# Kernel optimization log

Hardware: AMD Instinct MI355X
Metric: run time of the kernel (lower is better)

The kernel has to match this reference:

```python
import jax, jax.numpy as jnp
import numpy as np

H = 128        # hidden_dim
NP = 512       # program nodes
NV = 50000     # voxel nodes
E = 800000     # cross edges (16 per voxel)
TAU = 1.0
SLOPE = 0.01   # LeakyReLU default negative slope


def setup_inputs() -> dict:
    key = jax.random.key(0)
    ks = jax.random.split(key, 12)
    s = 1.0 / np.sqrt(H)
    x = jax.random.normal(ks[0], (NP, H), dtype=jnp.float32)
    v = jax.random.normal(ks[1], (NV, H), dtype=jnp.float32)
    row0 = jax.random.randint(ks[2], (E,), 0, NP, dtype=jnp.int32)
    row1 = (jnp.arange(E, dtype=jnp.int32) % NV)  # every voxel gets E/NV edges
    cross_edge_index = jnp.stack([row0, row1])    # [2, E]
    W_program = jax.random.normal(ks[3], (H, H), dtype=jnp.float32) * s
    b_program = jnp.zeros((H,), dtype=jnp.float32)
    W_voxel = jax.random.normal(ks[4], (H, H), dtype=jnp.float32) * s
    b_voxel = jnp.zeros((H,), dtype=jnp.float32)
    W_m1 = jax.random.normal(ks[5], (H, H), dtype=jnp.float32) * s
    b_m1 = jnp.zeros((H,), dtype=jnp.float32)
    W_m2 = jax.random.normal(ks[6], (H, 1), dtype=jnp.float32) * s
    b_m2 = jnp.zeros((1,), dtype=jnp.float32)
    theta = jax.random.normal(ks[7], (H, 1), dtype=jnp.float32) * s  # xavier-like
    u = jax.random.uniform(ks[8], (E,), dtype=jnp.float32)
    gumbel_u = jnp.clip(u, 1e-7, 1.0 - 1e-7)  # avoid log(0)
    return {"x": x, "v": v, "cross_edge_index": cross_edge_index,
            "W_program": W_program, "b_program": b_program,
            "W_voxel": W_voxel, "b_voxel": b_voxel,
            "W_m1": W_m1, "b_m1": b_m1, "W_m2": W_m2, "b_m2": b_m2,
            "theta": theta, "gumbel_u": gumbel_u}


def reference(x, v, cross_edge_index, W_program, b_program, W_voxel, b_voxel,
              W_m1, b_m1, W_m2, b_m2, theta, gumbel_u):
    src = cross_edge_index[0]
    dst = cross_edge_index[1]
    x_sel = x[src]                      # [E, H] gather
    v_sel = v[dst]                      # [E, H] gather
    # mask = sigmoid(MLP(v)) : Linear -> LeakyReLU -> Linear(H,1)
    a = v @ W_m1 + b_m1
    a = jnp.where(a >= 0, a, SLOPE * a)
    mask = jax.nn.sigmoid(a @ W_m2 + b_m2)                  # [NV, 1]
    # attention logits: theta^T * tanh(Wp x_sel + Wv v_sel), summed over H
    t = jnp.tanh(x_sel @ W_program + b_program + v_sel @ W_voxel + b_voxel)
    e = jnp.sum(t * theta[:, 0], axis=-1)                   # [E]
    # Gumbel softmax: global softmax over all edges (dim=0 in torch on 1-D e)
    g = -jnp.log(-jnp.log(gumbel_u))
    y = jax.nn.softmax((e + g) / TAU)                       # [E]
    # per-voxel hard argmax (scatter_max), straight-through estimator
    seg_max = jax.ops.segment_max(y, dst, num_segments=NV)  # [NV]
    is_max = y == seg_max[dst]
    cand = jnp.where(is_max, jnp.arange(E), E)
    argmax = jax.ops.segment_min(cand, dst, num_segments=NV)  # [NV], first max per voxel
    y_hard_1 = jnp.zeros(E + 1, y.dtype).at[argmax].set(1.0)[:E]  # overflow slot for empty segments
    y_hard = jax.lax.stop_gradient(y_hard_1 - y) + y
    # scatter-sum of soft-attended program features back to voxels
    summed = jax.ops.segment_sum(x_sel * y[:, None], dst, num_segments=NV)  # [NV, H]
    v_out = v + mask * summed
    return (v_out, mask, y[:, None], y_hard[:, None])
```

## Files before the change

### kernel.cpp

```cpp
#include <hip/hip_runtime.h>

#define H     128
#define NP    512
#define NVOX  50000
#define NEDGE 800000
#define EPV   16
#define SLOPE 0.01f
#define GR    32
#define NBLK  1563
#define STRH  136
#define VSTR  132
#define C1    2.8853900817779268f
#define LOG2E 1.4426950408889634f
#define ABLK  3125

#define EXP2(x) __builtin_amdgcn_exp2f(x)
#define LOG2(x) __builtin_amdgcn_logf(x)
#define RCP(x)  __builtin_amdgcn_rcpf(x)

typedef _Float16 h16;
typedef __attribute__((ext_vector_type(4))) _Float16 h16x4;
typedef __attribute__((ext_vector_type(8))) _Float16 h16x8;
typedef __attribute__((ext_vector_type(4))) float    f32x4;

__global__ __launch_bounds__(256) void k_pre(const float* __restrict__ x,
                                             const float* __restrict__ Wp,
                                             const float* __restrict__ bp,
                                             const float* __restrict__ Wv,
                                             const float* __restrict__ Wm1,
                                             float* __restrict__ xpout,
                                             h16* __restrict__ WvThi,
                                             h16* __restrict__ WvTlo,
                                             h16* __restrict__ Wm1T) {
    __shared__ float part[H];
    int bid = blockIdx.x;
    int tid = threadIdx.x;
    if (bid < NP) {
        int row = bid;
        int col = tid & 127;
        int kh  = tid >> 7;
        int kbase = kh * 64;
        const float* xr = x + (size_t)row * H;
        float acc = 0.f;
#pragma unroll 8
        for (int k = 0; k < 64; ++k)
            acc = fmaf(xr[kbase + k], Wp[(size_t)(kbase + k) * H + col], acc);
        if (kh == 1) part[col] = acc;
        __syncthreads();
        if (kh == 0) xpout[(size_t)row * H + col] = (acc + part[col] + bp[col]) * C1;
    } else {
        int idx = (bid - NP) * 256 + tid;
        if (idx < 16384) {
            int k = idx >> 7, n = idx & 127;
            float w = Wv[idx];
            h16 hi = (h16)w;
            WvThi[n * H + k] = hi;
            WvTlo[n * H + k] = (h16)(w - (float)hi);
        } else {
            int j = idx - 16384;
            int k = j >> 7, n = j & 127;
            Wm1T[n * H + k] = (h16)Wm1[j];
        }
    }
}

__global__ __launch_bounds__(256, 4) void k_mainX(
    const float* __restrict__ v,   const float* __restrict__ x,
    const float* __restrict__ bv,  const float* __restrict__ bm1,
    const float* __restrict__ Wm2, const float* __restrict__ bm2,
    const h16* __restrict__ WvThi, const h16* __restrict__ WvTlo,
    const h16* __restrict__ Wm1T,
    const float* __restrict__ xp,  const int* __restrict__ cei,
    const float* __restrict__ theta, const float* __restrict__ gum,
    float* __restrict__ mask_out, float* __restrict__ pout,
    float* __restrict__ sump,     float* __restrict__ partial)
{
    __shared__ __align__(16) char ldsbuf[2 * GR * STRH * 2];
    h16*   vh = (h16*)ldsbuf;
    h16*   vl = vh + GR * STRH;
    float* vt = (float*)ldsbuf;
    __shared__ float ptile[EPV * GR];
    __shared__ int   ceit[EPV * GR];
    __shared__ float gumt[EPV * GR];
    __shared__ int   amtile[GR];
    __shared__ float pmbuf[4][GR];
    __shared__ float psums[4];

    int tid  = threadIdx.x;
    int base = blockIdx.x * GR;

#pragma unroll
    for (int i = 0; i < 4; ++i) {
        int f  = i * 256 + tid;
        int r  = f >> 5, c4 = f & 31;
        int gr = base + r; if (gr >= NVOX) gr = NVOX - 1;
        float4 val = *(const float4*)&v[(size_t)gr * H + c4 * 4];
        h16x4 hi, lo;
        hi.x = (h16)val.x; lo.x = (h16)(val.x - (float)hi.x);
        hi.y = (h16)val.y; lo.y = (h16)(val.y - (float)hi.y);
        hi.z = (h16)val.z; lo.z = (h16)(val.z - (float)hi.z);
        hi.w = (h16)val.w; lo.w = (h16)(val.w - (float)hi.w);
        *(h16x4*)&vh[r * STRH + c4 * 4] = hi;
        *(h16x4*)&vl[r * STRH + c4 * 4] = lo;
    }
#pragma unroll
    for (int it = 0; it < 2; ++it) {
        int idx = it * 256 + tid;
        int t = idx >> 5, c = idx & 31;
        int vx = base + c; if (vx >= NVOX) vx = NVOX - 1;
        int e = vx + t * NVOX;
        ceit[idx] = cei[e];
        gumt[idx] = gum[e];
    }
    __syncthreads();

    int wave = tid >> 6, lane = tid & 63;
    int m16 = lane & 15, quad = lane >> 4;
    int cb = wave * 32;

    f32x4 aV[2][2], aM[2][2];
#pragma unroll
    for (int rt = 0; rt < 2; ++rt)
#pragma unroll
        for (int ct = 0; ct < 2; ++ct) { aV[rt][ct] = (f32x4)0.f; aM[rt][ct] = (f32x4)0.f; }

#pragma unroll
    for (int kc = 0; kc < 4; ++kc) {
        int kofs = kc * 32 + quad * 8;
        h16x8 ah[2], al[2];
#pragma unroll
        for (int rt = 0; rt < 2; ++rt) {
            int row = rt * 16 + m16;
            ah[rt] = *(const h16x8*)&vh[row * STRH + kofs];
            al[rt] = *(const h16x8*)&vl[row * STRH + kofs];
        }
#pragma unroll
        for (int ct = 0; ct < 2; ++ct) {
            int n = cb + ct * 16 + m16;
            h16x8 bh = *(const h16x8*)&WvThi[n * H + kofs];
            h16x8 bl = *(const h16x8*)&WvTlo[n * H + kofs];
            h16x8 bm = *(const h16x8*)&Wm1T[n * H + kofs];
#pragma unroll
            for (int rt = 0; rt < 2; ++rt) {
                aV[rt][ct] = __builtin_amdgcn_mfma_f32_16x16x32_f16(ah[rt], bh, aV[rt][ct], 0, 0, 0);
                aV[rt][ct] = __builtin_amdgcn_mfma_f32_16x16x32_f16(al[rt], bh, aV[rt][ct], 0, 0, 0);
                aV[rt][ct] = __builtin_amdgcn_mfma_f32_16x16x32_f16(ah[rt], bl, aV[rt][ct], 0, 0, 0);
                aM[rt][ct] = __builtin_amdgcn_mfma_f32_16x16x32_f16(ah[rt], bm, aM[rt][ct], 0, 0, 0);
            }
        }
    }
    __syncthreads();

    float pml[2][4];
#pragma unroll
    for (int rt = 0; rt < 2; ++rt)
#pragma unroll
        for (int reg = 0; reg < 4; ++reg) pml[rt][reg] = 0.f;
#pragma unroll
    for (int ct = 0; ct < 2; ++ct) {
        int col = cb + ct * 16 + m16;
        float bvc = bv[col], bmc = bm1[col], w2c = Wm2[col];
#pragma unroll
        for (int rt = 0; rt < 2; ++rt)
#pragma unroll
            for (int reg = 0; reg < 4; ++reg) {
                int row = rt * 16 + quad * 4 + reg;
                vt[row * VSTR + col] = (aV[rt][ct][reg] + bvc) * C1;
                float m = aM[rt][ct][reg] + bmc;
                m = (m >= 0.f) ? m : SLOPE * m;
                pml[rt][reg] = fmaf(m, w2c, pml[rt][reg]);
            }
    }
#pragma unroll
    for (int off = 8; off >= 1; off >>= 1)
#pragma unroll
        for (int rt = 0; rt < 2; ++rt)
#pragma unroll
            for (int reg = 0; reg < 4; ++reg)
                pml[rt][reg] += __shfl_xor(pml[rt][reg], off, 64);
    if (m16 == 0) {
#pragma unroll
        for (int rt = 0; rt < 2; ++rt)
#pragma unroll
            for (int reg = 0; reg < 4; ++reg)
                pmbuf[wave][rt * 16 + quad * 4 + reg] = pml[rt][reg];
    }
    __syncthreads();
    if (wave == 0 && lane < GR) {
        int gr = base + lane;
        if (gr < NVOX) {
            float s = pmbuf[0][lane] + pmbuf[1][lane] + pmbuf[2][lane]
                    + pmbuf[3][lane] + bm2[0];
            mask_out[gr] = RCP(1.f + EXP2(-s * LOG2E));
        }
    }

    int g = tid >> 3, lk = tid & 7;
    int vox = base + g;
    bool valid = vox < NVOX;
    float th2[16], thsum = 0.f;
#pragma unroll
    for (int i = 0; i < 4; ++i) {
        float4 t4 = *(const float4*)&theta[(lk + 8 * i) * 4];
        th2[i * 4 + 0] = -2.f * LOG2E * t4.x; th2[i * 4 + 1] = -2.f * LOG2E * t4.y;
        th2[i * 4 + 2] = -2.f * LOG2E * t4.z; th2[i * 4 + 3] = -2.f * LOG2E * t4.w;
        thsum += LOG2E * (t4.x + t4.y + t4.z + t4.w);
    }
    const float* vr = &vt[g * VSTR];
    float4 b0 = *(const float4*)&vr[(lk +  0) * 4];
    float4 b1 = *(const float4*)&vr[(lk +  8) * 4];
    float4 b2 = *(const float4*)&vr[(lk + 16) * 4];
    float4 b3 = *(const float4*)&vr[(lk + 24) * 4];

    float4 s0 = make_float4(0.f,0.f,0.f,0.f), s1 = s0, s2 = s0, s3 = s0;
    float psum = 0.f, pmax = -1.f;
    int   pidx = 0;

    int srcC = ceit[g];
    const float4* xr0 = (const float4*)(xp + (size_t)srcC * H);
    float4 a0 = xr0[lk], a1 = xr0[lk + 8], a2 = xr0[lk + 16], a3 = xr0[lk + 24];

    for (int t = 0; t < EPV; ++t) {
        float4 n0, n1, n2, n3;
        int srcN;
        if (t < EPV - 1) {
            srcN = ceit[(t + 1) * GR + g];
            const float4* xrN = (const float4*)(xp + (size_t)srcN * H);
            n0 = xrN[lk]; n1 = xrN[lk + 8]; n2 = xrN[lk + 16]; n3 = xrN[lk + 24];
        } else {
            srcN = srcC; n0 = a0; n1 = a1; n2 = a2; n3 = a3;
        }
        const float4* xo = (const float4*)(x + (size_t)srcC * H);
        float4 c0 = xo[lk], c1 = xo[lk + 8], c2 = xo[lk + 16], c3 = xo[lk + 24];
        float wvt = -LOG2E * RCP(LOG2(gumt[t * GR + g]));

        float acc0 = thsum, acc1 = 0.f;
        acc0 = fmaf(th2[ 0], RCP(EXP2(a0.x + b0.x) + 1.f), acc0);
        acc1 = fmaf(th2[ 1], RCP(EXP2(a0.y + b0.y) + 1.f), acc1);
        acc0 = fmaf(th2[ 2], RCP(EXP2(a0.z + b0.z) + 1.f), acc0);
        acc1 = fmaf(th2[ 3], RCP(EXP2(a0.w + b0.w) + 1.f), acc1);
        acc0 = fmaf(th2[ 4], RCP(EXP2(a1.x + b1.x) + 1.f), acc0);
        acc1 = fmaf(th2[ 5], RCP(EXP2(a1.y + b1.y) + 1.f), acc1);
        acc0 = fmaf(th2[ 6], RCP(EXP2(a1.z + b1.z) + 1.f), acc0);
        acc1 = fmaf(th2[ 7], RCP(EXP2(a1.w + b1.w) + 1.f), acc1);
        acc0 = fmaf(th2[ 8], RCP(EXP2(a2.x + b2.x) + 1.f), acc0);
        acc1 = fmaf(th2[ 9], RCP(EXP2(a2.y + b2.y) + 1.f), acc1);
        acc0 = fmaf(th2[10], RCP(EXP2(a2.z + b2.z) + 1.f), acc0);
        acc1 = fmaf(th2[11], RCP(EXP2(a2.w + b2.w) + 1.f), acc1);
        acc0 = fmaf(th2[12], RCP(EXP2(a3.x + b3.x) + 1.f), acc0);
        acc1 = fmaf(th2[13], RCP(EXP2(a3.y + b3.y) + 1.f), acc1);
        acc0 = fmaf(th2[14], RCP(EXP2(a3.z + b3.z) + 1.f), acc0);
        acc1 = fmaf(th2[15], RCP(EXP2(a3.w + b3.w) + 1.f), acc1);
        float acc = acc0 + acc1;
        acc += __shfl_xor(acc, 4, 64);
        acc += __shfl_xor(acc, 2, 64);
        acc += __shfl_xor(acc, 1, 64);
        float p = EXP2(acc) * wvt;
        if (p > pmax) { pmax = p; pidx = t; }
        if (valid) psum += p;
        if (lk == 0) ptile[t * GR + g] = p;
        s0.x = fmaf(p, c0.x, s0.x); s0.y = fmaf(p, c0.y, s0.y);
        s0.z = fmaf(p, c0.z, s0.z); s0.w = fmaf(p, c0.w, s0.w);
        s1.x = fmaf(p, c1.x, s1.x); s1.y = fmaf(p, c1.y, s1.y);
        s1.z = fmaf(p, c1.z, s1.z); s1.w = fmaf(p, c1.w, s1.w);
        s2.x = fmaf(p, c2.x, s2.x); s2.y = fmaf(p, c2.y, s2.y);
        s2.z = fmaf(p, c2.z, s2.z); s2.w = fmaf(p, c2.w, s2.w);
        s3.x = fmaf(p, c3.x, s3.x); s3.y = fmaf(p, c3.y, s3.y);
        s3.z = fmaf(p, c3.z, s3.z); s3.w = fmaf(p, c3.w, s3.w);
        a0 = n0; a1 = n1; a2 = n2; a3 = n3; srcC = srcN;
    }
    if (lk == 0) amtile[g] = pidx;
    if (valid) {
        float* sr = sump + (size_t)vox * H;
        *(float4*)&sr[(lk +  0) * 4] = s0;
        *(float4*)&sr[(lk +  8) * 4] = s1;
        *(float4*)&sr[(lk + 16) * 4] = s2;
        *(float4*)&sr[(lk + 24) * 4] = s3;
    }
    psum += __shfl_xor(psum, 8, 64);
    psum += __shfl_xor(psum, 16, 64);
    psum += __shfl_xor(psum, 32, 64);
    if (lane == 0) psums[wave] = psum;
    __syncthreads();
#pragma unroll
    for (int it = 0; it < 2; ++it) {
        int idx = it * 256 + tid;
        int t = idx >> 5, c = idx & 31;
        int vox2 = base + c;
        if (vox2 < NVOX) {
            float val = ptile[t * GR + c];
            pout[vox2 + t * NVOX] = (t == amtile[c]) ? -val : val;
        }
    }
    if (tid == 0)
        partial[blockIdx.x] = psums[0] + psums[1] + psums[2] + psums[3];
}

__global__ __launch_bounds__(256) void k_out(const float* __restrict__ v,
                                             const float* __restrict__ maskp,
                                             const float* __restrict__ partial,
                                             float* __restrict__ vout,
                                             float* __restrict__ ybuf,
                                             float* __restrict__ yhard) {
    __shared__ float wsum[4];
    int tid = threadIdx.x;
    float s = 0.f;
    for (int i = tid; i < NBLK; i += 256) s += partial[i];
#pragma unroll
    for (int off = 32; off >= 1; off >>= 1) s += __shfl_xor(s, off, 64);
    if ((tid & 63) == 0) wsum[tid >> 6] = s;
    __syncthreads();
    float invS = RCP(wsum[0] + wsum[1] + wsum[2] + wsum[3]);

    int bid = blockIdx.x;
    if (bid < ABLK) {
#pragma unroll
        for (int r = 0; r < 2; ++r) {
            int i = (bid + r * ABLK) * 256 + tid;
            float4 sp = ((const float4*)vout)[i];
            float4 vv = ((const float4*)v)[i];
            float  m  = maskp[i >> 5] * invS;
            float4 o;
            o.x = fmaf(m, sp.x, vv.x); o.y = fmaf(m, sp.y, vv.y);
            o.z = fmaf(m, sp.z, vv.z); o.w = fmaf(m, sp.w, vv.w);
            ((float4*)vout)[i] = o;
        }
    } else {
        int e = (bid - ABLK) * 256 + tid;
        float pv = ybuf[e];
        ybuf[e]  = fabsf(pv) * invS;
        yhard[e] = (pv < 0.f) ? 1.f : 0.f;
    }
}

extern "C" void kernel_launch(void* const* d_in, const int* in_sizes, int n_in,
                              void* d_out, int out_size, void* d_ws, size_t ws_size,
                              hipStream_t stream) {
    (void)in_sizes; (void)n_in; (void)out_size; (void)ws_size;
    const float* x   = (const float*)d_in[0];
    const float* v   = (const float*)d_in[1];
    const int*   cei = (const int*)d_in[2];
    const float* Wp  = (const float*)d_in[3];
    const float* bp  = (const float*)d_in[4];
    const float* Wv  = (const float*)d_in[5];
    const float* bv  = (const float*)d_in[6];
    const float* Wm1 = (const float*)d_in[7];
    const float* bm1 = (const float*)d_in[8];
    const float* Wm2 = (const float*)d_in[9];
    const float* bm2 = (const float*)d_in[10];
    const float* th  = (const float*)d_in[11];
    const float* gum = (const float*)d_in[12];

    float* out   = (float*)d_out;
    float* vout  = out;
    float* maskp = out + (size_t)NVOX * H;
    float* ybuf  = maskp + NVOX;
    float* yhard = ybuf + NEDGE;
    float* xp    = yhard;
    h16*   WvThi = (h16*)(yhard + 65536);
    h16*   WvTlo = WvThi + 16384;
    h16*   Wm1T  = WvThi + 32768;
    float* partial = (float*)d_ws;

    k_pre<<<NP + 128, 256, 0, stream>>>(x, Wp, bp, Wv, Wm1, xp, WvThi, WvTlo, Wm1T);
    k_mainX<<<NBLK, 256, 0, stream>>>(v, x, bv, bm1, Wm2, bm2, WvThi, WvTlo, Wm1T,
                                      xp, cei, th, gum, maskp, ybuf, vout, partial);
    k_out<<<2 * ABLK, 256, 0, stream>>>(v, maskp, partial, vout, ybuf, yhard);
}
```

Before: 180.8 us.

## Use DPP reductions, hoist gumbel log into staging, write p directly, raise occupancy

Several independent tweaks in the main kernel. Cross-lane shuffle reductions become DPP row operations, and the gumbel transform (log, reciprocal) moves from the edge loop into the LDS staging loop. Per-edge probabilities are written straight to global memory rather than through an LDS tile, with the argmax slot overwritten afterwards by -pmax, which removes the ptile/amtile buffers and the final write-out pass. The launch-bounds occupancy hint goes from 4 to 7 blocks per CU, which may force register spills. The direct stores are strided per voxel group, so coalescing is worse than the old tiled write-out.

```diff
diff --git a/kernel.cpp b/kernel.cpp
--- a/kernel.cpp
+++ b/kernel.cpp
@@ -22,6 +22,14 @@
 typedef __attribute__((ext_vector_type(4))) _Float16 h16x4;
 typedef __attribute__((ext_vector_type(8))) _Float16 h16x8;
 typedef __attribute__((ext_vector_type(4))) float    f32x4;
+
+template <int CTRL>
+__device__ __forceinline__ float dpp_add(float x) {
+    union { float f; int i; } u, r;
+    u.f = x;
+    r.i = __builtin_amdgcn_update_dpp(0, u.i, CTRL, 0xf, 0xf, true);
+    return x + r.f;
+}
 
 __global__ __launch_bounds__(256) void k_pre(const float* __restrict__ x,
                                              const float* __restrict__ Wp,
@@ -64,7 +72,7 @@
     }
 }
 
-__global__ __launch_bounds__(256, 4) void k_mainX(
+__global__ __launch_bounds__(256, 7) void k_mainX(
     const float* __restrict__ v,   const float* __restrict__ x,
     const float* __restrict__ bv,  const float* __restrict__ bm1,
     const float* __restrict__ Wm2, const float* __restrict__ bm2,
@@ -79,10 +87,8 @@
     h16*   vh = (h16*)ldsbuf;
     h16*   vl = vh + GR * STRH;
     float* vt = (float*)ldsbuf;
-    __shared__ float ptile[EPV * GR];
     __shared__ int   ceit[EPV * GR];
     __shared__ float gumt[EPV * GR];
-    __shared__ int   amtile[GR];
     __shared__ float pmbuf[4][GR];
     __shared__ float psums[4];
 
@@ -110,7 +116,7 @@
         int vx = base + c; if (vx >= NVOX) vx = NVOX - 1;
         int e = vx + t * NVOX;
         ceit[idx] = cei[e];
-        gumt[idx] = gum[e];
+        gumt[idx] = -LOG2E * RCP(LOG2(gum[e]));
     }
     __syncthreads();
 
@@ -172,12 +178,14 @@
             }
     }
 #pragma unroll
-    for (int off = 8; off >= 1; off >>= 1)
-#pragma unroll
-        for (int rt = 0; rt < 2; ++rt)
-#pragma unroll
-            for (int reg = 0; reg < 4; ++reg)
-                pml[rt][reg] += __shfl_xor(pml[rt][reg], off, 64);
+    for (int rt = 0; rt < 2; ++rt)
+#pragma unroll
+        for (int reg = 0; reg < 4; ++reg) {
+            pml[rt][reg] = dpp_add<0xB1>(pml[rt][reg]);
+            pml[rt][reg] = dpp_add<0x4E>(pml[rt][reg]);
+            pml[rt][reg] = dpp_add<0x141>(pml[rt][reg]);
+            pml[rt][reg] = dpp_add<0x140>(pml[rt][reg]);
+        }
     if (m16 == 0) {
 #pragma unroll
         for (int rt = 0; rt < 2; ++rt)
@@ -232,7 +240,7 @@
         }
         const float4* xo = (const float4*)(x + (size_t)srcC * H);
         float4 c0 = xo[lk], c1 = xo[lk + 8], c2 = xo[lk + 16], c3 = xo[lk + 24];
-        float wvt = -LOG2E * RCP(LOG2(gumt[t * GR + g]));
+        float wvt = gumt[t * GR + g];
 
         float acc0 = thsum, acc1 = 0.f;
         acc0 = fmaf(th2[ 0], RCP(EXP2(a0.x + b0.x) + 1.f), acc0);
@@ -252,13 +260,13 @@
         acc0 = fmaf(th2[14], RCP(EXP2(a3.z + b3.z) + 1.f), acc0);
         acc1 = fmaf(th2[15], RCP(EXP2(a3.w + b3.w) + 1.f), acc1);
         float acc = acc0 + acc1;
-        acc += __shfl_xor(acc, 4, 64);
-        acc += __shfl_xor(acc, 2, 64);
-        acc += __shfl_xor(acc, 1, 64);
+        acc = dpp_add<0xB1>(acc);
+        acc = dpp_add<0x4E>(acc);
+        acc = dpp_add<0x141>(acc);
         float p = EXP2(acc) * wvt;
         if (p > pmax) { pmax = p; pidx = t; }
         if (valid) psum += p;
-        if (lk == 0) ptile[t * GR + g] = p;
+        if (lk == 0 && valid) pout[vox + t * NVOX] = p;
         s0.x = fmaf(p, c0.x, s0.x); s0.y = fmaf(p, c0.y, s0.y);
         s0.z = fmaf(p, c0.z, s0.z); s0.w = fmaf(p, c0.w, s0.w);
         s1.x = fmaf(p, c1.x, s1.x); s1.y = fmaf(p, c1.y, s1.y);
@@ -269,7 +277,7 @@
         s3.z = fmaf(p, c3.z, s3.z); s3.w = fmaf(p, c3.w, s3.w);
         a0 = n0; a1 = n1; a2 = n2; a3 = n3; srcC = srcN;
     }
-    if (lk == 0) amtile[g] = pidx;
+    if (lk == 0 && valid) pout[vox + pidx * NVOX] = -pmax;
     if (valid) {
         float* sr = sump + (size_t)vox * H;
         *(float4*)&sr[(lk +  0) * 4] = s0;
@@ -282,16 +290,6 @@
     psum += __shfl_xor(psum, 32, 64);
     if (lane == 0) psums[wave] = psum;
     __syncthreads();
-#pragma unroll
-    for (int it = 0; it < 2; ++it) {
-        int idx = it * 256 + tid;
-        int t = idx >> 5, c = idx & 31;
-        int vox2 = base + c;
-        if (vox2 < NVOX) {
-            float val = ptile[t * GR + c];
-            pout[vox2 + t * NVOX] = (t == amtile[c]) ? -val : val;
-        }
-    }
     if (tid == 0)
         partial[blockIdx.x] = psums[0] + psums[1] + psums[2] + psums[3];
 }
```

Result: slower. 295.7 us (+63.6%).
